# Kernel tuning notes

Hardware: AMD Instinct MI355X
Metric: run time of the kernel (lower is better)

The kernel has to match this reference:

```python
import jax, jax.numpy as jnp
import numpy as np

GRID_NUM = 28
IMG_SIZE = 224.0
GRID_SIZE = IMG_SIZE / GRID_NUM
LAMBDA_COORD = 5.0
LAMBDA_NOOBJ = 0.5
NUM_CLASSES = 20
EPS = 1e-12


def setup_inputs() -> dict:
    key = jax.random.key(0)
    k1, k2, k3 = jax.random.split(key, 3)
    B, S = 1024, GRID_NUM
    y_pred = jax.random.uniform(k1, (B, S, S, 30), dtype=jnp.float32)
    # y_true channel 0: class id in {0..20}; 0 means no object. channels 1:5: (x, y, w, h)
    cls = jax.random.randint(k2, (B, S, S, 1), 0, NUM_CLASSES + 1).astype(jnp.float32)
    box = jax.random.uniform(k3, (B, S, S, 4), dtype=jnp.float32)
    y_true = jnp.concatenate([cls, box], axis=-1)
    return {"y_pred": y_pred, "y_true": y_true}


def _corners(box, gi, gj):
    # box[..., 0:2] are cell-relative center offsets, box[..., 2:4] are image-relative w/h
    cx = (gj + box[..., 0]) * GRID_SIZE
    cy = (gi + box[..., 1]) * GRID_SIZE
    w = box[..., 2] * IMG_SIZE
    h = box[..., 3] * IMG_SIZE
    return cx - w / 2, cy - h / 2, cx + w / 2, cy + h / 2


def _iou(box_a, box_b, gi, gj):
    ax1, ay1, ax2, ay2 = _corners(box_a, gi, gj)
    bx1, by1, bx2, by2 = _corners(box_b, gi, gj)
    iw = jnp.maximum(jnp.minimum(ax2, bx2) - jnp.maximum(ax1, bx1), 0.0)
    ih = jnp.maximum(jnp.minimum(ay2, by2) - jnp.maximum(ay1, by1), 0.0)
    inter = iw * ih
    area_a = jnp.maximum(ax2 - ax1, 0.0) * jnp.maximum(ay2 - ay1, 0.0)
    area_b = jnp.maximum(bx2 - bx1, 0.0) * jnp.maximum(by2 - by1, 0.0)
    return inter / (area_a + area_b - inter + EPS)


def reference(y_pred, y_true):
    B, S = y_pred.shape[0], y_pred.shape[1]
    gi = jnp.arange(S, dtype=jnp.float32)[None, :, None]  # broadcast over (B, S, S)
    gj = jnp.arange(S, dtype=jnp.float32)[None, None, :]

    obj_mask = y_true[..., 0] != 0.0  # (B, S, S)
    true_box = y_true[..., 1:5]

    iou0 = _iou(y_pred[..., 0:4], true_box, gi, gj)
    iou1 = _iou(y_pred[..., 5:9], true_box, gi, gj)
    # original: choose 0 iff iou0 > iou1, else 1
    choose1 = ~(iou0 > iou1)

    conf_pred = jnp.where(choose1, y_pred[..., 9], y_pred[..., 4])
    conf_true = jnp.where(choose1, iou1, iou0)
    xy_pred = jnp.where(choose1[..., None], y_pred[..., 5:7], y_pred[..., 0:2])

    loss_conf_obj = jnp.square(conf_pred - conf_true)
    loss_coord = LAMBDA_COORD * jnp.sum(jnp.square(xy_pred - y_true[..., 1:3]), axis=-1)

    cls_idx = y_true[..., 0].astype(jnp.int32) - 1
    cls_onehot = jax.nn.one_hot(cls_idx, NUM_CLASSES, dtype=y_pred.dtype)
    loss_cls = jnp.sum(jnp.square(y_pred[..., 10:] - cls_onehot), axis=-1)

    loss_conf_noobj = LAMBDA_NOOBJ * (jnp.square(y_pred[..., 4]) + jnp.square(y_pred[..., 9]))

    bsz = jnp.float32(B)
    loss_confidence = jnp.sum(jnp.where(obj_mask, loss_conf_obj, loss_conf_noobj)) / bsz
    loss_coordinate = jnp.sum(jnp.where(obj_mask, loss_coord, 0.0)) / bsz
    loss_classification = jnp.sum(jnp.where(obj_mask, loss_cls, 0.0)) / bsz
    return loss_confidence + loss_coordinate + loss_classification
```

## Files before the change

kernel.cpp:

```cpp
#include <hip/hip_runtime.h>


#define S_GRID 28
#define N_CELLS (1024 * S_GRID * S_GRID)
#define CPB 256

__device__ __forceinline__ float iou_calc(float bx, float by, float bw, float bh,
                                          float tx, float ty, float tw, float th,
                                          float gi, float gj) {
    float acx = (gj + bx) * 8.0f;
    float acy = (gi + by) * 8.0f;
    float aw  = bw * 224.0f;
    float ah  = bh * 224.0f;
    float ax1 = acx - aw * 0.5f, ax2 = acx + aw * 0.5f;
    float ay1 = acy - ah * 0.5f, ay2 = acy + ah * 0.5f;
    float bcx = (gj + tx) * 8.0f;
    float bcy = (gi + ty) * 8.0f;
    float btw = tw * 224.0f;
    float bth = th * 224.0f;
    float bx1 = bcx - btw * 0.5f, bx2 = bcx + btw * 0.5f;
    float by1 = bcy - bth * 0.5f, by2 = bcy + bth * 0.5f;

    float iw = fmaxf(fminf(ax2, bx2) - fmaxf(ax1, bx1), 0.0f);
    float ih = fmaxf(fminf(ay2, by2) - fmaxf(ay1, by1), 0.0f);
    float inter = iw * ih;
    float area_a = fmaxf(ax2 - ax1, 0.0f) * fmaxf(ay2 - ay1, 0.0f);
    float area_b = fmaxf(bx2 - bx1, 0.0f) * fmaxf(by2 - by1, 0.0f);
    return inter / (area_a + area_b - inter + 1e-12f);
}

__global__ void zero_out_kernel(float* out) {
    out[0] = 0.0f;
}

__global__ __launch_bounds__(256) void yolo_loss_kernel(const float4* __restrict__ yp4,
                                                        const float4* __restrict__ yt4,
                                                        float* __restrict__ out) {
    __shared__ float sp[CPB * 31];
    __shared__ __align__(16) float st[CPB * 5];

    int tid = threadIdx.x;
    int bcell = blockIdx.x * CPB;

    const float4* pb = yp4 + (size_t)blockIdx.x * (CPB * 30 / 4);
#pragma unroll
    for (int k = 0; k < 8; ++k) {
        int idx = k * 256 + tid;
        if (idx < 1920) {
            float4 v = pb[idx];
            int e = idx * 4;
            float vals[4] = {v.x, v.y, v.z, v.w};
#pragma unroll
            for (int j = 0; j < 4; ++j) {
                int ee = e + j;
                int cell = ee / 30;
                int rem = ee - cell * 30;
                sp[cell * 31 + rem] = vals[j];
            }
        }
    }

    const float4* tb = yt4 + (size_t)blockIdx.x * (CPB * 5 / 4);
#pragma unroll
    for (int k = 0; k < 2; ++k) {
        int idx = k * 256 + tid;
        if (idx < 320) {
            ((float4*)st)[idx] = tb[idx];
        }
    }

    __syncthreads();

    int c = bcell + tid;
    int ij = c % (S_GRID * S_GRID);
    float gi = (float)(ij / S_GRID);
    float gj = (float)(ij % S_GRID);

    float pr[30];
#pragma unroll
    for (int k = 0; k < 30; ++k) pr[k] = sp[tid * 31 + k];

    float tc = st[tid * 5 + 0];
    float tx = st[tid * 5 + 1];
    float ty = st[tid * 5 + 2];
    float tw = st[tid * 5 + 3];
    float th = st[tid * 5 + 4];

    float iou0 = iou_calc(pr[0], pr[1], pr[2], pr[3], tx, ty, tw, th, gi, gj);
    float iou1 = iou_calc(pr[5], pr[6], pr[7], pr[8], tx, ty, tw, th, gi, gj);
    bool choose1 = !(iou0 > iou1);

    float conf_pred = choose1 ? pr[9] : pr[4];
    float conf_true = choose1 ? iou1 : iou0;
    float xp = choose1 ? pr[5] : pr[0];
    float yp = choose1 ? pr[6] : pr[1];

    float dcf = conf_pred - conf_true;
    float loss_conf_obj = dcf * dcf;

    float d0 = xp - tx, d1 = yp - ty;
    float loss_coord = 5.0f * (d0 * d0 + d1 * d1);

    int cls = (int)tc - 1;
    float lcls = 0.0f;
#pragma unroll
    for (int k = 0; k < 20; ++k) {
        float oh = (k == cls) ? 1.0f : 0.0f;
        float d = pr[10 + k] - oh;
        lcls += d * d;
    }

    float loss_noobj = 0.5f * (pr[4] * pr[4] + pr[9] * pr[9]);

    bool obj = (tc != 0.0f);
    float val = obj ? (loss_conf_obj + loss_coord + lcls) : loss_noobj;

#pragma unroll
    for (int off = 32; off > 0; off >>= 1) {
        val += __shfl_down(val, off, 64);
    }
    __shared__ float wsum[4];
    int lane = tid & 63;
    int wid  = tid >> 6;
    if (lane == 0) wsum[wid] = val;
    __syncthreads();
    if (tid == 0) {
        float s = wsum[0] + wsum[1] + wsum[2] + wsum[3];
        atomicAdd(out, s * (1.0f / 1024.0f));
    }
}

extern "C" void kernel_launch(void* const* d_in, const int* in_sizes, int n_in,
                              void* d_out, int out_size, void* d_ws, size_t ws_size,
                              hipStream_t stream) {
    const float4* y_pred = (const float4*)d_in[0];
    const float4* y_true = (const float4*)d_in[1];
    float* out = (float*)d_out;

    zero_out_kernel<<<1, 1, 0, stream>>>(out);
    int blocks = N_CELLS / CPB;
    yolo_loss_kernel<<<blocks, 256, 0, stream>>>(y_pred, y_true, out);
}
```

Measured before the change: 175.4 us.

## Compute class loss during load, stage only box channels, two-pass reduction

The class and no-object loss terms are now accumulated directly from the coalesced float4 loads, and only the first 10 channels per cell are staged in shared memory. This shrinks LDS from 31 to 11 floats per cell. All global loads are issued up front before the first barrier, and IoU work runs only for object cells. The per-block atomicAdd plus zero kernel is replaced by per-block partials written to workspace and summed by a single-block reduce kernel. This adds a second launch and per-element division and branching in the load loop.

```diff
diff --git a/kernel.cpp b/kernel.cpp
--- a/kernel.cpp
+++ b/kernel.cpp
@@ -4,6 +4,7 @@
 #define S_GRID 28
 #define N_CELLS (1024 * S_GRID * S_GRID)
 #define CPB 256
+#define NBLOCKS (N_CELLS / CPB)
 
 __device__ __forceinline__ float iou_calc(float bx, float by, float bw, float bh,
                                           float tx, float ty, float tw, float th,
@@ -29,104 +30,129 @@
     return inter / (area_a + area_b - inter + 1e-12f);
 }
 
-__global__ void zero_out_kernel(float* out) {
-    out[0] = 0.0f;
-}
-
 __global__ __launch_bounds__(256) void yolo_loss_kernel(const float4* __restrict__ yp4,
                                                         const float4* __restrict__ yt4,
-                                                        float* __restrict__ out) {
-    __shared__ float sp[CPB * 31];
+                                                        float* __restrict__ partials) {
+    __shared__ float sp[CPB * 11];
     __shared__ __align__(16) float st[CPB * 5];
+    __shared__ float wsum[4];
 
     int tid = threadIdx.x;
-    int bcell = blockIdx.x * CPB;
 
-    const float4* pb = yp4 + (size_t)blockIdx.x * (CPB * 30 / 4);
+    const float4* tb = yt4 + (size_t)blockIdx.x * 320;
+    float4 vt0 = tb[tid];
+    float4 vt1 = (tid < 64) ? tb[256 + tid] : make_float4(0, 0, 0, 0);
+
+    const float4* pb = yp4 + (size_t)blockIdx.x * 1920;
+    float4 vp[8];
+#pragma unroll
+    for (int k = 0; k < 8; ++k) {
+        int idx = k * 256 + tid;
+        vp[k] = (idx < 1920) ? pb[idx] : make_float4(0, 0, 0, 0);
+    }
+
+    ((float4*)st)[tid] = vt0;
+    if (tid < 64) ((float4*)st)[256 + tid] = vt1;
+    __syncthreads();
+
+    float acc = 0.0f;
 #pragma unroll
     for (int k = 0; k < 8; ++k) {
         int idx = k * 256 + tid;
         if (idx < 1920) {
-            float4 v = pb[idx];
-            int e = idx * 4;
-            float vals[4] = {v.x, v.y, v.z, v.w};
+            float vals[4] = {vp[k].x, vp[k].y, vp[k].z, vp[k].w};
+            int e0 = idx * 4;
 #pragma unroll
             for (int j = 0; j < 4; ++j) {
-                int ee = e + j;
-                int cell = ee / 30;
-                int rem = ee - cell * 30;
-                sp[cell * 31 + rem] = vals[j];
+                int ee = e0 + j;
+                int lcell = ee / 30;
+                int ch = ee - lcell * 30;
+                float tc = st[lcell * 5];
+                bool obj = (tc != 0.0f);
+                float v = vals[j];
+                if (ch >= 10) {
+                    int cls = (int)tc - 1;
+                    float oh = (ch - 10 == cls) ? 1.0f : 0.0f;
+                    float d = v - oh;
+                    acc += obj ? d * d : 0.0f;
+                } else {
+                    sp[lcell * 11 + ch] = v;
+                    if (ch == 4 || ch == 9) {
+                        acc += obj ? 0.0f : 0.5f * v * v;
+                    }
+                }
             }
         }
     }
+    __syncthreads();
 
-    const float4* tb = yt4 + (size_t)blockIdx.x * (CPB * 5 / 4);
-#pragma unroll
-    for (int k = 0; k < 2; ++k) {
-        int idx = k * 256 + tid;
-        if (idx < 320) {
-            ((float4*)st)[idx] = tb[idx];
+    {
+        int c = blockIdx.x * CPB + tid;
+        int ij = c % (S_GRID * S_GRID);
+        float gi = (float)(ij / S_GRID);
+        float gj = (float)(ij % S_GRID);
+
+        float p0 = sp[tid * 11 + 0], p1 = sp[tid * 11 + 1];
+        float p2 = sp[tid * 11 + 2], p3 = sp[tid * 11 + 3];
+        float p4 = sp[tid * 11 + 4], p5 = sp[tid * 11 + 5];
+        float p6 = sp[tid * 11 + 6], p7 = sp[tid * 11 + 7];
+        float p8 = sp[tid * 11 + 8], p9 = sp[tid * 11 + 9];
+
+        float tc = st[tid * 5 + 0];
+        float tx = st[tid * 5 + 1];
+        float ty = st[tid * 5 + 2];
+        float tw = st[tid * 5 + 3];
+        float th = st[tid * 5 + 4];
+
+        if (tc != 0.0f) {
+            float iou0 = iou_calc(p0, p1, p2, p3, tx, ty, tw, th, gi, gj);
+            float iou1 = iou_calc(p5, p6, p7, p8, tx, ty, tw, th, gi, gj);
+            bool choose1 = !(iou0 > iou1);
+
+            float conf_pred = choose1 ? p9 : p4;
+            float conf_true = choose1 ? iou1 : iou0;
+            float xp = choose1 ? p5 : p0;
+            float yp = choose1 ? p6 : p1;
+
+            float dcf = conf_pred - conf_true;
+            float d0 = xp - tx, d1 = yp - ty;
+            acc += dcf * dcf + 5.0f * (d0 * d0 + d1 * d1);
         }
     }
 
-    __syncthreads();
-
-    int c = bcell + tid;
-    int ij = c % (S_GRID * S_GRID);
-    float gi = (float)(ij / S_GRID);
-    float gj = (float)(ij % S_GRID);
-
-    float pr[30];
-#pragma unroll
-    for (int k = 0; k < 30; ++k) pr[k] = sp[tid * 31 + k];
-
-    float tc = st[tid * 5 + 0];
-    float tx = st[tid * 5 + 1];
-    float ty = st[tid * 5 + 2];
-    float tw = st[tid * 5 + 3];
-    float th = st[tid * 5 + 4];
-
-    float iou0 = iou_calc(pr[0], pr[1], pr[2], pr[3], tx, ty, tw, th, gi, gj);
-    float iou1 = iou_calc(pr[5], pr[6], pr[7], pr[8], tx, ty, tw, th, gi, gj);
-    bool choose1 = !(iou0 > iou1);
-
-    float conf_pred = choose1 ? pr[9] : pr[4];
-    float conf_true = choose1 ? iou1 : iou0;
-    float xp = choose1 ? pr[5] : pr[0];
-    float yp = choose1 ? pr[6] : pr[1];
-
-    float dcf = conf_pred - conf_true;
-    float loss_conf_obj = dcf * dcf;
-
-    float d0 = xp - tx, d1 = yp - ty;
-    float loss_coord = 5.0f * (d0 * d0 + d1 * d1);
-
-    int cls = (int)tc - 1;
-    float lcls = 0.0f;
-#pragma unroll
-    for (int k = 0; k < 20; ++k) {
-        float oh = (k == cls) ? 1.0f : 0.0f;
-        float d = pr[10 + k] - oh;
-        lcls += d * d;
-    }
-
-    float loss_noobj = 0.5f * (pr[4] * pr[4] + pr[9] * pr[9]);
-
-    bool obj = (tc != 0.0f);
-    float val = obj ? (loss_conf_obj + loss_coord + lcls) : loss_noobj;
-
 #pragma unroll
     for (int off = 32; off > 0; off >>= 1) {
-        val += __shfl_down(val, off, 64);
+        acc += __shfl_down(acc, off, 64);
+    }
+    int lane = tid & 63;
+    int wid  = tid >> 6;
+    if (lane == 0) wsum[wid] = acc;
+    __syncthreads();
+    if (tid == 0) {
+        partials[blockIdx.x] = wsum[0] + wsum[1] + wsum[2] + wsum[3];
+    }
+}
+
+__global__ __launch_bounds__(256) void reduce_kernel(const float* __restrict__ partials,
+                                                     float* __restrict__ out) {
+    int tid = threadIdx.x;
+    float s = 0.0f;
+#pragma unroll
+    for (int k = 0; k < 13; ++k) {
+        int i = k * 256 + tid;
+        if (i < NBLOCKS) s += partials[i];
+    }
+#pragma unroll
+    for (int off = 32; off > 0; off >>= 1) {
+        s += __shfl_down(s, off, 64);
     }
     __shared__ float wsum[4];
     int lane = tid & 63;
     int wid  = tid >> 6;
-    if (lane == 0) wsum[wid] = val;
+    if (lane == 0) wsum[wid] = s;
     __syncthreads();
     if (tid == 0) {
-        float s = wsum[0] + wsum[1] + wsum[2] + wsum[3];
-        atomicAdd(out, s * (1.0f / 1024.0f));
+        out[0] = (wsum[0] + wsum[1] + wsum[2] + wsum[3]) * (1.0f / 1024.0f);
     }
 }
 
@@ -136,8 +162,8 @@
     const float4* y_pred = (const float4*)d_in[0];
     const float4* y_true = (const float4*)d_in[1];
     float* out = (float*)d_out;
+    float* partials = (float*)d_ws;
 
-    zero_out_kernel<<<1, 1, 0, stream>>>(out);
-    int blocks = N_CELLS / CPB;
-    yolo_loss_kernel<<<blocks, 256, 0, stream>>>(y_pred, y_true, out);
+    yolo_loss_kernel<<<NBLOCKS, 256, 0, stream>>>(y_pred, y_true, partials);
+    reduce_kernel<<<1, 256, 0, stream>>>(partials, out);
 }
```

New measurement: 158.0 us. 1.11x faster.

## Use direct global-to-LDS loads, smaller blocks, and two-pass partial reduction

Applied to the files above, without the earlier changes.

Loads the prediction tile straight into LDS with the global_load_lds builtin, replacing per-element scattered LDS stores into a padded layout. Block size drops to 128 cells, so there are more blocks. Each block now writes a partial sum to the workspace and a single-block kernel reduces them, which removes the per-block float atomics and the zeroing kernel. The unpadded 30-stride LDS layout can cause bank conflicts on the per-thread reads, and the extra reduce launch adds a small serial tail.

```diff
diff --git a/kernel.cpp b/kernel.cpp
--- a/kernel.cpp
+++ b/kernel.cpp
@@ -3,7 +3,11 @@
 
 #define S_GRID 28
 #define N_CELLS (1024 * S_GRID * S_GRID)
-#define CPB 256
+#define CPB 128
+#define NBLOCKS (N_CELLS / CPB)
+
+typedef const __attribute__((address_space(1))) unsigned int* gptr_t;
+typedef __attribute__((address_space(3))) unsigned int* lptr_t;
 
 __device__ __forceinline__ float iou_calc(float bx, float by, float bw, float bh,
                                           float tx, float ty, float tw, float th,
@@ -29,56 +33,46 @@
     return inter / (area_a + area_b - inter + 1e-12f);
 }
 
-__global__ void zero_out_kernel(float* out) {
-    out[0] = 0.0f;
-}
+__global__ __launch_bounds__(128) void yolo_loss_kernel(const float4* __restrict__ yp4,
+                                                        const float4* __restrict__ yt4,
+                                                        float* __restrict__ partials) {
+    __shared__ float sp[CPB * 30];
+    __shared__ __align__(16) float st[CPB * 5];
+    __shared__ float wsum[2];
 
-__global__ __launch_bounds__(256) void yolo_loss_kernel(const float4* __restrict__ yp4,
-                                                        const float4* __restrict__ yt4,
-                                                        float* __restrict__ out) {
-    __shared__ float sp[CPB * 31];
-    __shared__ __align__(16) float st[CPB * 5];
-
-    int tid = threadIdx.x;
-    int bcell = blockIdx.x * CPB;
+    int tid  = threadIdx.x;
+    int lane = tid & 63;
+    int wave = tid >> 6;
 
     const float4* pb = yp4 + (size_t)blockIdx.x * (CPB * 30 / 4);
 #pragma unroll
     for (int k = 0; k < 8; ++k) {
-        int idx = k * 256 + tid;
-        if (idx < 1920) {
-            float4 v = pb[idx];
-            int e = idx * 4;
-            float vals[4] = {v.x, v.y, v.z, v.w};
-#pragma unroll
-            for (int j = 0; j < 4; ++j) {
-                int ee = e + j;
-                int cell = ee / 30;
-                int rem = ee - cell * 30;
-                sp[cell * 31 + rem] = vals[j];
-            }
+        int c = k * 2 + wave;
+        if (c < 15) {
+            const float4* src = pb + c * 64 + lane;
+            __builtin_amdgcn_global_load_lds((gptr_t)src,
+                                             (lptr_t)(sp + c * 256),
+                                             16, 0, 0);
         }
     }
 
     const float4* tb = yt4 + (size_t)blockIdx.x * (CPB * 5 / 4);
-#pragma unroll
-    for (int k = 0; k < 2; ++k) {
-        int idx = k * 256 + tid;
-        if (idx < 320) {
-            ((float4*)st)[idx] = tb[idx];
-        }
-    }
+    float4 v0 = tb[tid];
+    float4 v1 = (tid < 32) ? tb[128 + tid] : make_float4(0, 0, 0, 0);
+    ((float4*)st)[tid] = v0;
+    if (tid < 32) ((float4*)st)[128 + tid] = v1;
 
     __syncthreads();
 
-    int c = bcell + tid;
+    int c = blockIdx.x * CPB + tid;
     int ij = c % (S_GRID * S_GRID);
     float gi = (float)(ij / S_GRID);
     float gj = (float)(ij % S_GRID);
 
     float pr[30];
+    const float* p = sp + tid * 30;
 #pragma unroll
-    for (int k = 0; k < 30; ++k) pr[k] = sp[tid * 31 + k];
+    for (int k = 0; k < 30; ++k) pr[k] = p[k];
 
     float tc = st[tid * 5 + 0];
     float tx = st[tid * 5 + 1];
@@ -96,10 +90,7 @@
     float yp = choose1 ? pr[6] : pr[1];
 
     float dcf = conf_pred - conf_true;
-    float loss_conf_obj = dcf * dcf;
-
     float d0 = xp - tx, d1 = yp - ty;
-    float loss_coord = 5.0f * (d0 * d0 + d1 * d1);
 
     int cls = (int)tc - 1;
     float lcls = 0.0f;
@@ -110,23 +101,41 @@
         lcls += d * d;
     }
 
-    float loss_noobj = 0.5f * (pr[4] * pr[4] + pr[9] * pr[9]);
-
-    bool obj = (tc != 0.0f);
-    float val = obj ? (loss_conf_obj + loss_coord + lcls) : loss_noobj;
+    float obj_loss   = dcf * dcf + 5.0f * (d0 * d0 + d1 * d1) + lcls;
+    float noobj_loss = 0.5f * (pr[4] * pr[4] + pr[9] * pr[9]);
+    float val = (tc != 0.0f) ? obj_loss : noobj_loss;
 
 #pragma unroll
     for (int off = 32; off > 0; off >>= 1) {
         val += __shfl_down(val, off, 64);
     }
+    if (lane == 0) wsum[wave] = val;
+    __syncthreads();
+    if (tid == 0) {
+        partials[blockIdx.x] = wsum[0] + wsum[1];
+    }
+}
+
+__global__ __launch_bounds__(256) void reduce_kernel(const float* __restrict__ partials,
+                                                     float* __restrict__ out) {
+    int tid = threadIdx.x;
+    float s = 0.0f;
+#pragma unroll
+    for (int k = 0; k < 25; ++k) {
+        int i = k * 256 + tid;
+        if (i < NBLOCKS) s += partials[i];
+    }
+#pragma unroll
+    for (int off = 32; off > 0; off >>= 1) {
+        s += __shfl_down(s, off, 64);
+    }
     __shared__ float wsum[4];
     int lane = tid & 63;
     int wid  = tid >> 6;
-    if (lane == 0) wsum[wid] = val;
+    if (lane == 0) wsum[wid] = s;
     __syncthreads();
     if (tid == 0) {
-        float s = wsum[0] + wsum[1] + wsum[2] + wsum[3];
-        atomicAdd(out, s * (1.0f / 1024.0f));
+        out[0] = (wsum[0] + wsum[1] + wsum[2] + wsum[3]) * (1.0f / 1024.0f);
     }
 }
 
@@ -136,8 +145,8 @@
     const float4* y_pred = (const float4*)d_in[0];
     const float4* y_true = (const float4*)d_in[1];
     float* out = (float*)d_out;
+    float* partials = (float*)d_ws;
 
-    zero_out_kernel<<<1, 1, 0, stream>>>(out);
-    int blocks = N_CELLS / CPB;
-    yolo_loss_kernel<<<blocks, 256, 0, stream>>>(y_pred, y_true, out);
+    yolo_loss_kernel<<<NBLOCKS, CPB, 0, stream>>>(y_pred, y_true, partials);
+    reduce_kernel<<<1, 256, 0, stream>>>(partials, out);
 }
```

After: 153.1 us. -12.7%, faster.
